# Performance work log

Hardware: AMD Instinct MI355X
Metric: run time of the kernel (lower is better)

Reference implementation:

```python
import jax, jax.numpy as jnp
import numpy as np


def setup_inputs() -> dict:
    key = jax.random.key(0)
    ks = jax.random.split(key, 7)
    b, t, c = 2, 2048, 1024
    s = 0.02  # keep pre-softmax logits in a sane range
    return {
        "query": jax.random.normal(ks[0], (b, t, c), jnp.float32),
        "key": jax.random.normal(ks[1], (b, t, c), jnp.float32),
        "value": jax.random.normal(ks[2], (b, t, c), jnp.float32),
        "in_proj_w": jax.random.normal(ks[3], (3 * c, c), jnp.float32) * s,
        "in_proj_b": jax.random.normal(ks[4], (3 * c,), jnp.float32) * s,
        "out_proj_w": jax.random.normal(ks[5], (c, c), jnp.float32) * s,
        "out_proj_b": jax.random.normal(ks[6], (c,), jnp.float32) * s,
        "window_size": 128,
    }


def reference(query, key, value, in_proj_w, in_proj_b, out_proj_w, out_proj_b, window_size):
    num_heads = 16
    b, t, c = query.shape
    hd = c // num_heads
    wq, wk, wv = in_proj_w[:c], in_proj_w[c:2 * c], in_proj_w[2 * c:]
    bq, bk, bv = in_proj_b[:c], in_proj_b[c:2 * c], in_proj_b[2 * c:]
    # project and split heads: [b, h, t, hd]
    q = (query @ wq.T + bq).reshape(b, t, num_heads, hd).transpose(0, 2, 1, 3)
    k = (key @ wk.T + bk).reshape(b, t, num_heads, hd).transpose(0, 2, 1, 3)
    v = (value @ wv.T + bv).reshape(b, t, num_heads, hd).transpose(0, 2, 1, 3)
    # NOTE: torch adds a *float* attn_mask to the logits. The original mask is
    # 1.0 inside the sliding window, 0.0 outside -- an additive +1 bias, NOT -inf.
    idx = jnp.arange(t)
    band = (jnp.abs(idx[:, None] - idx[None, :]) <= window_size).astype(q.dtype)  # [t, t]
    scale = 1.0 / jnp.sqrt(jnp.asarray(hd, q.dtype))
    logits = jnp.einsum("bhqd,bhkd->bhqk", q * scale, k) + band  # [b,h,t,t]
    attn = jax.nn.softmax(logits, axis=-1)
    out = jnp.einsum("bhqk,bhkd->bhqd", attn, v)  # [b,h,t,hd]
    out = out.transpose(0, 2, 1, 3).reshape(b, t, c)
    return out @ out_proj_w.T + out_proj_b
```

## Files before the change

kernel.cpp:

```cpp
#include <hip/hip_runtime.h>

typedef __attribute__((ext_vector_type(8)))  short short8;
typedef __attribute__((ext_vector_type(4)))  float f32x4;
typedef __attribute__((ext_vector_type(16))) float f32x16;

constexpr int B  = 2;
constexpr int T  = 2048;
constexpr int C  = 1024;
constexpr int H  = 16;
constexpr int HD = 64;

__device__ inline unsigned bf16rne(float a){
  unsigned u = __builtin_bit_cast(unsigned, a);
  u += 0x7fffu + ((u >> 16) & 1u);
  return u >> 16;
}
__device__ inline unsigned bf16pair(float a, float b){
  unsigned ua = __builtin_bit_cast(unsigned, a); ua += 0x7fffu + ((ua >> 16) & 1u);
  unsigned ub = __builtin_bit_cast(unsigned, b); ub += 0x7fffu + ((ub >> 16) & 1u);
  return (ua >> 16) | (ub & 0xffff0000u);
}
__device__ inline void gll16(const void* g, void* l){
  __builtin_amdgcn_global_load_lds(
      (const __attribute__((address_space(1))) unsigned*)g,
      (__attribute__((address_space(3))) unsigned*)l, 16, 0, 0);
}
__device__ inline float exp2f_(float x){
#if __has_builtin(__builtin_amdgcn_exp2f)
  return __builtin_amdgcn_exp2f(x);
#else
  return __builtin_exp2f(x);
#endif
}

__global__ void convert_k(const float* __restrict__ ipw, const float* __restrict__ opw,
                          const float* __restrict__ q, const float* __restrict__ k,
                          const float* __restrict__ v, unsigned* __restrict__ dst)
{
  const int i = blockIdx.x * 256 + threadIdx.x;
  const long e = (long)i * 4;
  const float* src; long off;
  if      (e <  3145728) { src = ipw; off = e; }
  else if (e <  4194304) { src = opw; off = e - 3145728; }
  else if (e <  8388608) { src = q;   off = e - 4194304; }
  else if (e < 12582912) { src = k;   off = e - 8388608; }
  else                   { src = v;   off = e - 12582912; }
  const float4 x = *(const float4*)(src + off);
  dst[i*2+0] = bf16pair(x.x, x.y);
  dst[i*2+1] = bf16pair(x.z, x.w);
}

__global__ __launch_bounds__(256, 3) void gemm_qkv(
    const unsigned short* __restrict__ A0, const unsigned short* __restrict__ A1,
    const unsigned short* __restrict__ A2,
    const unsigned short* __restrict__ Wb, const float* __restrict__ bias,
    unsigned short* __restrict__ Qb, unsigned short* __restrict__ Kf,
    unsigned short* __restrict__ Vf)
{
  __shared__ __align__(16) char gsm[18944];
  unsigned short* As = (unsigned short*)gsm;
  unsigned short* Bs = (unsigned short*)(gsm + 8192);

  const int tid  = threadIdx.x, lane = tid & 63, wv = tid >> 6;
  const int wm   = wv & 1, wn = wv >> 1;
  const int bn   = blockIdx.x, bm = blockIdx.y;
  const int m16  = lane & 15, quad = lane >> 4;

  const int which = bn >> 3;
  const unsigned short* A = (which == 0) ? A0 : (which == 1 ? A1 : A2);

  f32x4 acc[4][4];
#pragma unroll
  for (int i = 0; i < 4; i++)
#pragma unroll
    for (int j = 0; j < 4; j++) acc[i][j] = (f32x4){0.f, 0.f, 0.f, 0.f};

  const int srow = wv * 32 + (lane >> 2);
  const int skp  = (lane & 3) * 8;

  for (int k0 = 0; k0 < 1024; k0 += 32) {
    __syncthreads();
#pragma unroll
    for (int p = 0; p < 2; p++) {
      gll16(A  + (size_t)(bm*128 + srow + p*16)*1024 + k0 + skp, (char*)As + wv*2048 + p*1024);
      gll16(Wb + (size_t)(bn*128 + srow + p*16)*1024 + k0 + skp, (char*)Bs + wv*2048 + p*1024);
    }
    __syncthreads();

    short8 af[4], bf[4];
#pragma unroll
    for (int i = 0; i < 4; i++)
      af[i] = *(const short8*)((const char*)As + (wm*64 + i*16 + m16)*64 + quad*16);
#pragma unroll
    for (int j = 0; j < 4; j++)
      bf[j] = *(const short8*)((const char*)Bs + (wn*64 + j*16 + m16)*64 + quad*16);
#pragma unroll
    for (int i = 0; i < 4; i++)
#pragma unroll
      for (int j = 0; j < 4; j++)
        acc[i][j] = __builtin_amdgcn_mfma_f32_16x16x32_bf16(af[i], bf[j], acc[i][j], 0,0,0);
  }

  __syncthreads();
  float* Ls = (float*)gsm;
  const int hbase = (bn & 7) * 2;
  const int b = bm >> 4;
  const int tbase = (bm & 15) * 128;
  const float ksc = (which == 1) ? 0.18033688f : 1.0f;

  if (which < 2) {
#pragma unroll
    for (int j = 0; j < 4; ++j) {
      const float bj = bias[bn*128 + wn*64 + j*16 + m16] * ksc;
#pragma unroll
      for (int i = 0; i < 4; ++i) {
        const int m0 = wm*64 + i*16 + quad*4;
#pragma unroll
        for (int r = 0; r < 4; ++r)
          Ls[(m0 + r)*36 + wn*16 + m16] = __builtin_fmaf(acc[i][j][r], ksc, bj);
      }
      __syncthreads();
#pragma unroll
      for (int r2 = 0; r2 < 2; ++r2) {
        const int v = r2*256 + tid;
        const int m = v & 127, seg = v >> 7;
        const int wn2 = seg >> 1;
        const float* src = &Ls[m*36 + wn2*16 + (seg & 1)*8];
        const float4 f0 = *(const float4*)src;
        const float4 f1 = *(const float4*)(src + 4);
        uint4 st;
        st.x = bf16pair(f0.x, f0.y); st.y = bf16pair(f0.z, f0.w);
        st.z = bf16pair(f1.x, f1.y); st.w = bf16pair(f1.z, f1.w);
        const int bhh = b*16 + hbase + wn2;
        if (which == 0) {
          const int d0 = j*16 + (seg & 1)*8;
          *(uint4*)&Qb[((size_t)(bhh*2048) + tbase + m)*64 + d0] = st;
        } else {
          const int kt = (tbase + m) >> 6;
          const int wkk = (m >> 5) & 1, ln2 = m & 31;
          const int h2 = seg & 1;
          uint4* dp = (uint4*)Kf + ((size_t)(bhh*32 + kt)*8 + j*2 + wkk)*64 + h2*32 + ln2;
          *dp = st;
        }
      }
      __syncthreads();
    }
  } else {
#pragma unroll
    for (int j = 0; j < 4; ++j) {
      const float bj = bias[bn*128 + wn*64 + j*16 + m16];
      const int col = wn*16 + m16;
#pragma unroll
      for (int i = 0; i < 4; ++i) {
        f32x4 tv = acc[i][j];
        tv[0] += bj; tv[1] += bj; tv[2] += bj; tv[3] += bj;
        *(f32x4*)&Ls[col*132 + wm*64 + i*16 + quad*4] = tv;
      }
      __syncthreads();
#pragma unroll
      for (int r2 = 0; r2 < 2; ++r2) {
        const int v = r2*256 + tid;
        const int n = v >> 4, mseg = v & 15;
        const float* src = &Ls[n*132 + mseg*8];
        const float4 f0 = *(const float4*)src;
        const float4 f1 = *(const float4*)(src + 4);
        uint4 st;
        st.x = bf16pair(f0.x, f0.y); st.y = bf16pair(f0.z, f0.w);
        st.z = bf16pair(f1.x, f1.y); st.w = bf16pair(f1.z, f1.w);
        const int d = j*16 + (n & 15);
        const int bhh = b*16 + hbase + (n >> 4);
        const int t0 = tbase + mseg*8;
        const int kt = t0 >> 6, tc = (t0 & 63) >> 3;
        const int wkk = tc >> 2, cc = (tc >> 1) & 1, h2 = tc & 1;
        const int dt = d >> 5, ln2 = d & 31;
        uint4* dp = (uint4*)Vf + (size_t)(bhh*32 + kt)*512 + dt*256 + cc*128 + wkk*64 + h2*32 + ln2;
        *dp = st;
      }
      __syncthreads();
    }
  }
}

__global__ __launch_bounds__(256, 3) void gemm_out(
    const unsigned short* __restrict__ Ab, const unsigned short* __restrict__ Wb,
    const float* __restrict__ bias, float* __restrict__ outF)
{
  __shared__ __align__(16) char gsm[12288];
  unsigned short* As = (unsigned short*)gsm;
  unsigned short* Ws = (unsigned short*)(gsm + 8192);

  const int tid  = threadIdx.x, lane = tid & 63, wv = tid >> 6;
  const int wm   = wv & 1, wn = wv >> 1;
  const int bn   = blockIdx.x, bm = blockIdx.y;
  const int m16  = lane & 15, quad = lane >> 4;

  f32x4 acc[4][2];
#pragma unroll
  for (int i = 0; i < 4; i++)
#pragma unroll
    for (int j = 0; j < 2; j++) acc[i][j] = (f32x4){0.f, 0.f, 0.f, 0.f};

  const int arow = wv * 32 + (lane >> 2);
  const int wrow = wv * 16 + (lane >> 2);
  const int skp  = (lane & 3) * 8;

  for (int k0 = 0; k0 < 1024; k0 += 32) {
    __syncthreads();
#pragma unroll
    for (int p = 0; p < 2; p++)
      gll16(Ab + (size_t)(bm*128 + arow + p*16)*1024 + k0 + skp, (char*)As + wv*2048 + p*1024);
    gll16(Wb + (size_t)(bn*64 + wrow)*1024 + k0 + skp, (char*)Ws + wv*1024);
    __syncthreads();

    short8 af[4], bf[2];
#pragma unroll
    for (int i = 0; i < 4; i++)
      af[i] = *(const short8*)((const char*)As + (wm*64 + i*16 + m16)*64 + quad*16);
#pragma unroll
    for (int j = 0; j < 2; j++)
      bf[j] = *(const short8*)((const char*)Ws + (wn*32 + j*16 + m16)*64 + quad*16);
#pragma unroll
    for (int i = 0; i < 4; i++)
#pragma unroll
      for (int j = 0; j < 2; j++)
        acc[i][j] = __builtin_amdgcn_mfma_f32_16x16x32_bf16(af[i], bf[j], acc[i][j], 0,0,0);
  }

#pragma unroll
  for (int j = 0; j < 2; j++) {
    const int n_e = bn*64 + wn*32 + j*16 + m16;
    const float bj = bias[n_e];
#pragma unroll
    for (int i = 0; i < 4; i++) {
      const int mbase = bm*128 + wm*64 + i*16 + quad*4;
#pragma unroll
      for (int r = 0; r < 4; r++)
        outF[(size_t)(mbase + r) * 1024 + n_e] = acc[i][j][r] + bj;
    }
  }
}

__global__ __launch_bounds__(256, 3) void attn_k(
    const unsigned short* __restrict__ Qb, const unsigned short* __restrict__ Kf,
    const unsigned short* __restrict__ Vf, const int* __restrict__ wptr,
    unsigned short* __restrict__ ctx)
{
  __shared__ __align__(16) char smem[16896];
  float* Om   = (float*)smem;
  float* lbuf = (float*)(smem + 16384);

  const int tid = threadIdx.x, lane = tid & 63, wv = tid >> 6;
  const int wq = wv >> 1, wk = wv & 1;
  const int h = lane >> 5, ln = lane & 31;
  const bool hs = (h == 1);
  const int bh = blockIdx.x, qt = blockIdx.y;
  const int win = *wptr;
  const int q0 = qt * 64 + wq * 32;
  const size_t hb = (size_t)bh * T * HD;

  constexpr float LOG2E = 1.44269504f;

  short8 qf[4];
#pragma unroll
  for (int s = 0; s < 4; s++)
    qf[s] = *(const short8*)(Qb + hb + (size_t)(q0 + ln)*64 + s*16 + h*8);

  short8 onesv;
#pragma unroll
  for (int jj = 0; jj < 8; jj++) onesv[jj] = (short)0x3F80;

  f32x16 O0, O1, Lacc, Zv;
#pragma unroll
  for (int r = 0; r < 16; r++) { O0[r] = 0.f; O1[r] = 0.f; Lacc[r] = 0.f; Zv[r] = 0.f; }
  const int tq = q0 + ln;

  const uint4* kbase = (const uint4*)Kf + (size_t)bh*32*512 + wk*64 + lane;
  const uint4* vbase = (const uint4*)Vf + (size_t)bh*32*512 + wk*64 + lane;

  uint4 kA[4], vA[4];
#pragma unroll
  for (int s = 0; s < 4; s++) kA[s] = kbase[s*128];
#pragma unroll
  for (int u = 0; u < 4; u++) vA[u] = vbase[(u >> 1)*256 + (u & 1)*128];

  for (int kt = 0; kt < 32; ++kt) {
    f32x16 st;
#pragma unroll
    for (int s = 0; s < 4; s++) {
      const short8 kf2 = __builtin_bit_cast(short8, kA[s]);
      st = __builtin_amdgcn_mfma_f32_32x32x16_bf16(kf2, qf[s], (s == 0 ? Zv : st), 0, 0, 0);
    }
    if (kt < 31) {
      const size_t o = (size_t)(kt + 1) * 512;
#pragma unroll
      for (int s = 0; s < 4; s++) kA[s] = kbase[o + s*128];
    }

    const int kb = kt*64 + wk*32;
    int sep = 0;
    if (kb > q0 + 31) sep = kb - (q0 + 31);
    else if (q0 > kb + 31) sep = q0 - (kb + 31);
    const int d1 = kb + 31 - q0, d2 = q0 + 31 - kb;
    const int dmax = max(d1 < 0 ? -d1 : d1, d2 < 0 ? -d2 : d2);

    float pr[16];
    if (sep > win) {
#pragma unroll
      for (int r = 0; r < 16; r++) pr[r] = exp2f_(st[r]);
    } else if (dmax <= win) {
#pragma unroll
      for (int r = 0; r < 16; r++) pr[r] = exp2f_(st[r] + LOG2E);
    } else {
      const int tkb = kb + 4*h;
#pragma unroll
      for (int r = 0; r < 16; r++) {
        const int tk = tkb + (r & 3) + 8*(r >> 2);
        int dd = tq - tk; dd = dd < 0 ? -dd : dd;
        pr[r] = exp2f_(st[r] + (dd <= win ? LOG2E : 0.0f));
      }
    }

    unsigned pk[8];
#pragma unroll
    for (int g = 0; g < 8; g++)
      pk[g] = __builtin_amdgcn_perm(__builtin_bit_cast(unsigned, pr[2*g+1]),
                                    __builtin_bit_cast(unsigned, pr[2*g]),
                                    0x07060302u);

#pragma unroll
    for (int c = 0; c < 2; c++) {
      const unsigned sh0 = (unsigned)__shfl_xor((int)pk[4*c+0], 32, 64);
      const unsigned sh1 = (unsigned)__shfl_xor((int)pk[4*c+1], 32, 64);
      const unsigned sh2 = (unsigned)__shfl_xor((int)pk[4*c+2], 32, 64);
      const unsigned sh3 = (unsigned)__shfl_xor((int)pk[4*c+3], 32, 64);
      union { unsigned u[4]; short8 v; } P;
      P.u[0] = hs ? sh2 : pk[4*c+0];
      P.u[1] = hs ? sh3 : pk[4*c+1];
      P.u[2] = hs ? pk[4*c+2] : sh0;
      P.u[3] = hs ? pk[4*c+3] : sh1;
#pragma unroll
      for (int dt = 0; dt < 2; dt++) {
        const short8 vf2 = __builtin_bit_cast(short8, vA[dt*2 + c]);
        if (dt == 0) O0 = __builtin_amdgcn_mfma_f32_32x32x16_bf16(P.v, vf2, O0, 0,0,0);
        else         O1 = __builtin_amdgcn_mfma_f32_32x32x16_bf16(P.v, vf2, O1, 0,0,0);
      }
      Lacc = __builtin_amdgcn_mfma_f32_32x32x16_bf16(P.v, onesv, Lacc, 0,0,0);
    }

    if (kt < 31) {
      const size_t o = (size_t)(kt + 1) * 512;
#pragma unroll
      for (int u = 0; u < 4; u++) vA[u] = vbase[o + (u >> 1)*256 + (u & 1)*128];
    }
  }

  __syncthreads();
  if (wk == 1) {
#pragma unroll
    for (int r = 0; r < 16; r++) {
      Om[wq*2048 + r*64 + lane]        = O0[r];
      Om[wq*2048 + (16 + r)*64 + lane] = O1[r];
    }
    if (ln == 0) {
#pragma unroll
      for (int r = 0; r < 16; r++)
        lbuf[wq*32 + (r & 3) + 8*(r >> 2) + 4*h] = Lacc[r];
    }
  }
  __syncthreads();
  if (wk == 0) {
    const int b = bh >> 4, hh = bh & 15;
#pragma unroll
    for (int r = 0; r < 16; r++) {
      const int qrow = (r & 3) + 8*(r >> 2) + 4*h;
      const float lt = Lacc[r] + lbuf[wq*32 + qrow];
      const float linv = 1.0f / lt;
      const int t = q0 + qrow;
      const float o0 = (O0[r] + Om[wq*2048 + r*64 + lane]) * linv;
      const float o1 = (O1[r] + Om[wq*2048 + (16 + r)*64 + lane]) * linv;
      unsigned short* cp = ctx + (size_t)(b*2048 + t)*1024 + hh*64;
      cp[ln]      = (unsigned short)bf16rne(o0);
      cp[32 + ln] = (unsigned short)bf16rne(o1);
    }
  }
}

extern "C" void kernel_launch(void* const* d_in, const int* in_sizes, int n_in,
                              void* d_out, int out_size, void* d_ws, size_t ws_size,
                              hipStream_t stream)
{
  const float* query = (const float*)d_in[0];
  const float* key   = (const float*)d_in[1];
  const float* value = (const float*)d_in[2];
  const float* ipw   = (const float*)d_in[3];
  const float* ipb   = (const float*)d_in[4];
  const float* opw   = (const float*)d_in[5];
  const float* opb   = (const float*)d_in[6];
  const int*   win   = (const int*)d_in[7];

  char* ws = (char*)d_ws;
  unsigned short* Winbf  = (unsigned short*)(ws);
  unsigned short* Woutbf = (unsigned short*)(ws + 6291456);
  unsigned short* Qin    = (unsigned short*)(ws + 8388608);
  unsigned short* Kin    = (unsigned short*)(ws + 16777216);
  unsigned short* Vin    = (unsigned short*)(ws + 25165824);
  unsigned short* Qb     = (unsigned short*)(ws + 33554432);
  unsigned short* Kf     = (unsigned short*)(ws + 41943040);
  unsigned short* Vf     = (unsigned short*)(ws + 50331648);
  unsigned short* ctx    = (unsigned short*)(ws + 58720256);

  convert_k<<<16384, 256, 0, stream>>>(ipw, opw, query, key, value, (unsigned*)ws);

  gemm_qkv<<<dim3(24, 32), 256, 0, stream>>>(
      Qin, Kin, Vin, Winbf, ipb, Qb, Kf, Vf);

  attn_k<<<dim3(32, 32), 256, 0, stream>>>(Qb, Kf, Vf, win, ctx);

  gemm_out<<<dim3(16, 32), 256, 0, stream>>>(
      ctx, Woutbf, opb, (float*)d_out);
}
```

Measured before the change: 225.2 us.

## Split attention key range four ways per 32-query tile and use permlane32 swap

Each attention block now handles 32 queries, and its four waves each process a quarter of the key tiles (16 iterations instead of 32). Partial O and row sums from three waves are reduced through shared memory by wave 0. The grid doubles and occupancy is raised to 4 blocks per SIMD. The intent is to shorten each wave's serial loop and expose more parallelism. The half-wave exchange of P now uses permlane32_swap instead of shfl_xor plus selects, and the reciprocal uses the fast rcp. The cost is more shared memory, a larger reduction step, and duplicate Q loads across waves.

After: 266.9 us. 18.5% more time.

```diff
diff --git a/kernel.cpp b/kernel.cpp
--- a/kernel.cpp
+++ b/kernel.cpp
@@ -3,6 +3,7 @@
 typedef __attribute__((ext_vector_type(8)))  short short8;
 typedef __attribute__((ext_vector_type(4)))  float f32x4;
 typedef __attribute__((ext_vector_type(16))) float f32x16;
+typedef __attribute__((ext_vector_type(2)))  unsigned uint2v;
 
 constexpr int B  = 2;
 constexpr int T  = 2048;
@@ -240,22 +241,20 @@
   }
 }
 
-__global__ __launch_bounds__(256, 3) void attn_k(
+__global__ __launch_bounds__(256, 4) void attn_k(
     const unsigned short* __restrict__ Qb, const unsigned short* __restrict__ Kf,
     const unsigned short* __restrict__ Vf, const int* __restrict__ wptr,
     unsigned short* __restrict__ ctx)
 {
-  __shared__ __align__(16) char smem[16896];
+  __shared__ __align__(16) char smem[25088];
   float* Om   = (float*)smem;
-  float* lbuf = (float*)(smem + 16384);
-
-  const int tid = threadIdx.x, lane = tid & 63, wv = tid >> 6;
-  const int wq = wv >> 1, wk = wv & 1;
+  float* lbuf = (float*)(smem + 24576);
+
+  const int tid = threadIdx.x, lane = tid & 63, wk = tid >> 6;
   const int h = lane >> 5, ln = lane & 31;
-  const bool hs = (h == 1);
   const int bh = blockIdx.x, qt = blockIdx.y;
   const int win = *wptr;
-  const int q0 = qt * 64 + wq * 32;
+  const int q0 = qt * 32;
   const size_t hb = (size_t)bh * T * HD;
 
   constexpr float LOG2E = 1.44269504f;
@@ -274,8 +273,8 @@
   for (int r = 0; r < 16; r++) { O0[r] = 0.f; O1[r] = 0.f; Lacc[r] = 0.f; Zv[r] = 0.f; }
   const int tq = q0 + ln;
 
-  const uint4* kbase = (const uint4*)Kf + (size_t)bh*32*512 + wk*64 + lane;
-  const uint4* vbase = (const uint4*)Vf + (size_t)bh*32*512 + wk*64 + lane;
+  const uint4* kbase = (const uint4*)Kf + (size_t)bh*16384 + (wk >> 1)*512 + (wk & 1)*64 + lane;
+  const uint4* vbase = (const uint4*)Vf + (size_t)bh*16384 + (wk >> 1)*512 + (wk & 1)*64 + lane;
 
   uint4 kA[4], vA[4];
 #pragma unroll
@@ -283,20 +282,20 @@
 #pragma unroll
   for (int u = 0; u < 4; u++) vA[u] = vbase[(u >> 1)*256 + (u & 1)*128];
 
-  for (int kt = 0; kt < 32; ++kt) {
+  for (int kt = 0; kt < 16; ++kt) {
     f32x16 st;
 #pragma unroll
     for (int s = 0; s < 4; s++) {
       const short8 kf2 = __builtin_bit_cast(short8, kA[s]);
       st = __builtin_amdgcn_mfma_f32_32x32x16_bf16(kf2, qf[s], (s == 0 ? Zv : st), 0, 0, 0);
     }
-    if (kt < 31) {
-      const size_t o = (size_t)(kt + 1) * 512;
+    if (kt < 15) {
+      const size_t o = (size_t)(kt + 1) * 1024;
 #pragma unroll
       for (int s = 0; s < 4; s++) kA[s] = kbase[o + s*128];
     }
 
-    const int kb = kt*64 + wk*32;
+    const int kb = kt*128 + wk*32;
     int sep = 0;
     if (kb > q0 + 31) sep = kb - (q0 + 31);
     else if (q0 > kb + 31) sep = q0 - (kb + 31);
@@ -329,15 +328,13 @@
 
 #pragma unroll
     for (int c = 0; c < 2; c++) {
-      const unsigned sh0 = (unsigned)__shfl_xor((int)pk[4*c+0], 32, 64);
-      const unsigned sh1 = (unsigned)__shfl_xor((int)pk[4*c+1], 32, 64);
-      const unsigned sh2 = (unsigned)__shfl_xor((int)pk[4*c+2], 32, 64);
-      const unsigned sh3 = (unsigned)__shfl_xor((int)pk[4*c+3], 32, 64);
+      const uint2v s02 = __builtin_amdgcn_permlane32_swap(pk[4*c+0], pk[4*c+2], false, false);
+      const uint2v s13 = __builtin_amdgcn_permlane32_swap(pk[4*c+1], pk[4*c+3], false, false);
       union { unsigned u[4]; short8 v; } P;
-      P.u[0] = hs ? sh2 : pk[4*c+0];
-      P.u[1] = hs ? sh3 : pk[4*c+1];
-      P.u[2] = hs ? pk[4*c+2] : sh0;
-      P.u[3] = hs ? pk[4*c+3] : sh1;
+      P.u[0] = s02[0];
+      P.u[1] = s13[0];
+      P.u[2] = s02[1];
+      P.u[3] = s13[1];
 #pragma unroll
       for (int dt = 0; dt < 2; dt++) {
         const short8 vf2 = __builtin_bit_cast(short8, vA[dt*2 + c]);
@@ -347,24 +344,24 @@
       Lacc = __builtin_amdgcn_mfma_f32_32x32x16_bf16(P.v, onesv, Lacc, 0,0,0);
     }
 
-    if (kt < 31) {
-      const size_t o = (size_t)(kt + 1) * 512;
+    if (kt < 15) {
+      const size_t o = (size_t)(kt + 1) * 1024;
 #pragma unroll
       for (int u = 0; u < 4; u++) vA[u] = vbase[o + (u >> 1)*256 + (u & 1)*128];
     }
   }
 
-  __syncthreads();
-  if (wk == 1) {
+  if (wk != 0) {
+    float* reg = Om + (wk - 1) * 2048;
 #pragma unroll
     for (int r = 0; r < 16; r++) {
-      Om[wq*2048 + r*64 + lane]        = O0[r];
-      Om[wq*2048 + (16 + r)*64 + lane] = O1[r];
+      reg[r*64 + lane]        = O0[r];
+      reg[(16 + r)*64 + lane] = O1[r];
     }
     if (ln == 0) {
 #pragma unroll
       for (int r = 0; r < 16; r++)
-        lbuf[wq*32 + (r & 3) + 8*(r >> 2) + 4*h] = Lacc[r];
+        lbuf[(wk - 1)*32 + (r & 3) + 8*(r >> 2) + 4*h] = Lacc[r];
     }
   }
   __syncthreads();
@@ -373,11 +370,13 @@
 #pragma unroll
     for (int r = 0; r < 16; r++) {
       const int qrow = (r & 3) + 8*(r >> 2) + 4*h;
-      const float lt = Lacc[r] + lbuf[wq*32 + qrow];
-      const float linv = 1.0f / lt;
+      const float lt = Lacc[r] + lbuf[qrow] + lbuf[32 + qrow] + lbuf[64 + qrow];
+      const float linv = __builtin_amdgcn_rcpf(lt);
       const int t = q0 + qrow;
-      const float o0 = (O0[r] + Om[wq*2048 + r*64 + lane]) * linv;
-      const float o1 = (O1[r] + Om[wq*2048 + (16 + r)*64 + lane]) * linv;
+      const float o0 = (O0[r] + Om[r*64 + lane] + Om[2048 + r*64 + lane]
+                              + Om[4096 + r*64 + lane]) * linv;
+      const float o1 = (O1[r] + Om[(16 + r)*64 + lane] + Om[2048 + (16 + r)*64 + lane]
+                              + Om[4096 + (16 + r)*64 + lane]) * linv;
       unsigned short* cp = ctx + (size_t)(b*2048 + t)*1024 + hh*64;
       cp[ln]      = (unsigned short)bf16rne(o0);
       cp[32 + ln] = (unsigned short)bf16rne(o1);
@@ -414,7 +413,7 @@
   gemm_qkv<<<dim3(24, 32), 256, 0, stream>>>(
       Qin, Kin, Vin, Winbf, ipb, Qb, Kf, Vf);
 
-  attn_k<<<dim3(32, 32), 256, 0, stream>>>(Qb, Kf, Vf, win, ctx);
+  attn_k<<<dim3(32, 64), 256, 0, stream>>>(Qb, Kf, Vf, win, ctx);
 
   gemm_out<<<dim3(16, 32), 256, 0, stream>>>(
       ctx, Woutbf, opb, (float*)d_out);
```
